# Kernel tuning notes

Measured on AMD Instinct MI355X. Metric: run time of the kernel, lower is better.

The kernel has to match this reference:

```python
import jax, jax.numpy as jnp
import numpy as np


def setup_inputs() -> dict:
    key = jax.random.key(0)
    ks = jax.random.split(key, 8)
    N, E, F, H = 50000, 400000, 128, 512
    x = jax.random.normal(ks[0], (N, F), dtype=jnp.float32)
    edge_index = jax.random.randint(ks[1], (2, E), 0, N, dtype=jnp.int32)
    W1 = jax.random.normal(ks[2], (H, 2 * F), dtype=jnp.float32) * 0.05
    b1 = jax.random.normal(ks[3], (H,), dtype=jnp.float32) * 0.05
    W2 = jax.random.normal(ks[4], (H, 2 * H), dtype=jnp.float32) * 0.05
    b2 = jax.random.normal(ks[5], (H,), dtype=jnp.float32) * 0.05
    Wo = jax.random.normal(ks[6], (1, H), dtype=jnp.float32) * 0.05
    bo = jax.random.normal(ks[7], (1,), dtype=jnp.float32) * 0.05
    return {"x": x, "edge_index": edge_index, "W1": W1, "b1": b1,
            "W2": W2, "b2": b2, "Wo": Wo, "bo": bo}


def reference(x, edge_index, W1, b1, W2, b2, Wo, bo):
    # GraphSAGE mean aggregation: agg[dst] = mean over incoming edges of h[src]
    N = x.shape[0]
    src = edge_index[0]
    dst = edge_index[1]
    deg = jax.ops.segment_sum(jnp.ones_like(dst, dtype=x.dtype), dst,
                              num_segments=N)
    inv_deg = 1.0 / jnp.maximum(deg, 1.0)  # clamp_min(1.0)

    def agg_mean(h):
        s = jax.ops.segment_sum(h[src], dst, num_segments=N)  # [N, D]
        return s * inv_deg[:, None]

    # Layer 1: concat(self, neigh) -> Linear -> ReLU (dropout = identity, eval)
    n1 = agg_mean(x)
    h1 = jax.nn.relu(jnp.concatenate([x, n1], axis=1) @ W1.T + b1)
    # Layer 2
    n2 = agg_mean(h1)
    h2 = jax.nn.relu(jnp.concatenate([h1, n2], axis=1) @ W2.T + b2)
    # Output head
    logits = h2 @ Wo.T + bo  # [N, 1]
    return jax.nn.sigmoid(logits)
```

## Files before the change

### kernel.cpp

```cpp
#include <hip/hip_runtime.h>
#include <math.h>


typedef __attribute__((ext_vector_type(8))) short bf16x8;
typedef __attribute__((ext_vector_type(4))) float f32x4;

static inline int ceil_div(int a, int b) { return (a + b - 1) / b; }

__device__ inline float bf2f_lo(unsigned u) { return __builtin_bit_cast(float, u << 16); }
__device__ inline float bf2f_hi(unsigned u) { return __builtin_bit_cast(float, u & 0xffff0000u); }
__device__ inline unsigned f2bf(float f) {
    unsigned u = __builtin_bit_cast(unsigned, f);
    u += 0x7fffu + ((u >> 16) & 1u);
    return u >> 16;
}

#define GLOAD_LDS16(gp, lp)                                                   \
    __builtin_amdgcn_global_load_lds(                                         \
        (__attribute__((address_space(1))) void*)(gp),                        \
        (__attribute__((address_space(3))) void*)(lp), 16, 0, 0)


__global__ void hist_kernel(const int* __restrict__ dst, int* __restrict__ deg, int E) {
    int e = blockIdx.x * 256 + threadIdx.x;
    if (e < E) atomicAdd(&deg[dst[e]], 1);
}

__global__ __launch_bounds__(256) void chunk_reduce(const int* __restrict__ deg,
                                                    int* __restrict__ partial, int N) {
    int base = blockIdx.x * 1024;
    int s = 0;
    for (int i = threadIdx.x; i < 1024; i += 256) {
        int idx = base + i;
        if (idx < N) s += deg[idx];
    }
    #pragma unroll
    for (int off = 32; off; off >>= 1) s += __shfl_down(s, off);
    __shared__ int ws[4];
    if ((threadIdx.x & 63) == 0) ws[threadIdx.x >> 6] = s;
    __syncthreads();
    if (threadIdx.x == 0) partial[blockIdx.x] = ws[0] + ws[1] + ws[2] + ws[3];
}

__global__ void partial_scan(int* __restrict__ partial, int* __restrict__ rowstartN, int P) {
    int lane = threadIdx.x;
    int v = (lane < P) ? partial[lane] : 0;
    int incl = v;
    #pragma unroll
    for (int off = 1; off < 64; off <<= 1) {
        int t = __shfl_up(incl, off);
        if (lane >= off) incl += t;
    }
    if (lane < P) partial[lane] = incl - v;
    if (lane == 63) *rowstartN = incl;
}

__global__ __launch_bounds__(256) void chunk_scan(const int* __restrict__ deg,
                                                  const int* __restrict__ partial,
                                                  int* __restrict__ rowstart,
                                                  int* __restrict__ cursor, int N) {
    int base = blockIdx.x * 1024 + threadIdx.x * 4;
    int v[4];
    #pragma unroll
    for (int j = 0; j < 4; ++j) {
        int i = base + j;
        v[j] = (i < N) ? deg[i] : 0;
    }
    int mysum = v[0] + v[1] + v[2] + v[3];
    int incl = mysum;
    int lane = threadIdx.x & 63, wave = threadIdx.x >> 6;
    #pragma unroll
    for (int off = 1; off < 64; off <<= 1) {
        int t = __shfl_up(incl, off);
        if (lane >= off) incl += t;
    }
    __shared__ int ws[4];
    if (lane == 63) ws[wave] = incl;
    __syncthreads();
    int run = partial[blockIdx.x] + incl - mysum;
    for (int w = 0; w < wave; ++w) run += ws[w];
    #pragma unroll
    for (int j = 0; j < 4; ++j) {
        int i = base + j;
        if (i < N) { rowstart[i] = run; cursor[i] = run; }
        run += v[j];
    }
}

__global__ void bucket_kernel(const int* __restrict__ src, const int* __restrict__ dst,
                              int* __restrict__ cursor, int* __restrict__ ebuf, int E) {
    int e = blockIdx.x * 256 + threadIdx.x;
    if (e < E) {
        int pos = atomicAdd(&cursor[dst[e]], 1);
        ebuf[pos] = src[e];
    }
}


__global__ void cvt_bf16_kernel(const float* __restrict__ in, unsigned short* __restrict__ out, int n4) {
    int i = blockIdx.x * 256 + threadIdx.x;
    if (i < n4) {
        float4 v = ((const float4*)in)[i];
        ushort4 o;
        o.x = (unsigned short)f2bf(v.x);
        o.y = (unsigned short)f2bf(v.y);
        o.z = (unsigned short)f2bf(v.z);
        o.w = (unsigned short)f2bf(v.w);
        ((ushort4*)out)[i] = o;
    }
}


__global__ void gather_mean_128(const int* __restrict__ rowstart, const int* __restrict__ ebuf,
                                const unsigned* __restrict__ featb, unsigned* __restrict__ outb, int N) {
    int w = (blockIdx.x * blockDim.x + threadIdx.x) >> 6;
    int lane = threadIdx.x & 63;
    if (w >= N) return;
    int e0 = rowstart[w], e1 = rowstart[w + 1];
    float ax = 0.0f, ay = 0.0f;
    int i = e0;
    for (; i + 4 <= e1; i += 4) {
        unsigned v0 = featb[(size_t)ebuf[i]     * 64 + lane];
        unsigned v1 = featb[(size_t)ebuf[i + 1] * 64 + lane];
        unsigned v2 = featb[(size_t)ebuf[i + 2] * 64 + lane];
        unsigned v3 = featb[(size_t)ebuf[i + 3] * 64 + lane];
        ax += bf2f_lo(v0) + bf2f_lo(v1) + bf2f_lo(v2) + bf2f_lo(v3);
        ay += bf2f_hi(v0) + bf2f_hi(v1) + bf2f_hi(v2) + bf2f_hi(v3);
    }
    for (; i < e1; ++i) {
        unsigned v = featb[(size_t)ebuf[i] * 64 + lane];
        ax += bf2f_lo(v); ay += bf2f_hi(v);
    }
    float inv = 1.0f / fmaxf((float)(e1 - e0), 1.0f);
    outb[(size_t)w * 64 + lane] = f2bf(ax * inv) | (f2bf(ay * inv) << 16);
}

__global__ void gather_mean_512(const int* __restrict__ rowstart, const int* __restrict__ ebuf,
                                const unsigned short* __restrict__ featb,
                                unsigned short* __restrict__ outb, int N) {
    int w = (blockIdx.x * blockDim.x + threadIdx.x) >> 6;
    int lane = threadIdx.x & 63;
    if (w >= N) return;
    int e0 = rowstart[w], e1 = rowstart[w + 1];
    float a[8] = {0, 0, 0, 0, 0, 0, 0, 0};
    const uint4* base = (const uint4*)featb;
    int i = e0;
    for (; i + 4 <= e1; i += 4) {
        uint4 v0 = base[(size_t)ebuf[i]     * 64 + lane];
        uint4 v1 = base[(size_t)ebuf[i + 1] * 64 + lane];
        uint4 v2 = base[(size_t)ebuf[i + 2] * 64 + lane];
        uint4 v3 = base[(size_t)ebuf[i + 3] * 64 + lane];
        a[0] += bf2f_lo(v0.x) + bf2f_lo(v1.x) + bf2f_lo(v2.x) + bf2f_lo(v3.x);
        a[1] += bf2f_hi(v0.x) + bf2f_hi(v1.x) + bf2f_hi(v2.x) + bf2f_hi(v3.x);
        a[2] += bf2f_lo(v0.y) + bf2f_lo(v1.y) + bf2f_lo(v2.y) + bf2f_lo(v3.y);
        a[3] += bf2f_hi(v0.y) + bf2f_hi(v1.y) + bf2f_hi(v2.y) + bf2f_hi(v3.y);
        a[4] += bf2f_lo(v0.z) + bf2f_lo(v1.z) + bf2f_lo(v2.z) + bf2f_lo(v3.z);
        a[5] += bf2f_hi(v0.z) + bf2f_hi(v1.z) + bf2f_hi(v2.z) + bf2f_hi(v3.z);
        a[6] += bf2f_lo(v0.w) + bf2f_lo(v1.w) + bf2f_lo(v2.w) + bf2f_lo(v3.w);
        a[7] += bf2f_hi(v0.w) + bf2f_hi(v1.w) + bf2f_hi(v2.w) + bf2f_hi(v3.w);
    }
    for (; i < e1; ++i) {
        uint4 v = base[(size_t)ebuf[i] * 64 + lane];
        a[0] += bf2f_lo(v.x); a[1] += bf2f_hi(v.x);
        a[2] += bf2f_lo(v.y); a[3] += bf2f_hi(v.y);
        a[4] += bf2f_lo(v.z); a[5] += bf2f_hi(v.z);
        a[6] += bf2f_lo(v.w); a[7] += bf2f_hi(v.w);
    }
    float inv = 1.0f / fmaxf((float)(e1 - e0), 1.0f);
    uint4 o;
    o.x = f2bf(a[0] * inv) | (f2bf(a[1] * inv) << 16);
    o.y = f2bf(a[2] * inv) | (f2bf(a[3] * inv) << 16);
    o.z = f2bf(a[4] * inv) | (f2bf(a[5] * inv) << 16);
    o.w = f2bf(a[6] * inv) | (f2bf(a[7] * inv) << 16);
    ((uint4*)outb)[(size_t)w * 64 + lane] = o;
}

__global__ __launch_bounds__(256) void gemm_mfma(
    const unsigned short* __restrict__ A0,
    const unsigned short* __restrict__ A1,
    const unsigned short* __restrict__ W,
    const float* __restrict__ b,
    unsigned short* __restrict__ outb,
    const float* __restrict__ Wo,
    float* __restrict__ logit,
    int N, int K0, int K1, int C, int mode)
{
    const int nrow = (N + 127) >> 7;
    const int id   = blockIdx.x;
    const int rowb = ((id >> 5) << 3) + (id & 7);
    const int colb = (id >> 3) & 3;
    if (rowb >= nrow) return;

    const int K = K0 + K1;
    const int S = K0;
    __shared__ short As[2][4096];
    __shared__ short Bs[2][4096];

    const int tid  = threadIdx.x;
    const int lane = tid & 63;
    const int wave = tid >> 6;
    const int wm = wave & 1, wn = wave >> 1;
    const int cl = lane & 15, quad = lane >> 4;
    const int row0 = rowb * 128;
    const int col0 = colb * 128;

    const int r = lane >> 2;
    const int j = lane & 3;
    const int trow0 = wave * 32 + r;
    const int trow1 = trow0 + 16;
    const int ar0 = (row0 + trow0 < N) ? row0 + trow0 : N - 1;
    const int ar1 = (row0 + trow1 < N) ? row0 + trow1 : N - 1;
    const size_t aoff0 = (size_t)ar0 * S + j * 8;
    const size_t aoff1 = (size_t)ar1 * S + j * 8;
    const size_t boff0 = (size_t)(col0 + trow0) * K + j * 8;
    const size_t boff1 = (size_t)(col0 + trow1) * K + j * 8;
    const int lds0 = (wave * 32) * 32;
    const int lds1 = (wave * 32 + 16) * 32;

    f32x4 acc[4][4];
    #pragma unroll
    for (int mt = 0; mt < 4; ++mt)
        #pragma unroll
        for (int nt = 0; nt < 4; ++nt)
            acc[mt][nt] = (f32x4){0.f, 0.f, 0.f, 0.f};

    GLOAD_LDS16(A0 + aoff0, &As[0][lds0]);
    GLOAD_LDS16(A0 + aoff1, &As[0][lds1]);
    GLOAD_LDS16(W  + boff0, &Bs[0][lds0]);
    GLOAD_LDS16(W  + boff1, &Bs[0][lds1]);

    const int iters = K >> 5;
    for (int i = 0; i < iters; ++i) {
        const int cur = i & 1;
        __syncthreads();
        if (i + 1 < iters) {
            const int kn = (i + 1) << 5;
            const unsigned short* Ab = (kn < K0) ? (A0 + kn) : (A1 + (kn - K0));
            const unsigned short* Wb = W + kn;
            const int nb = cur ^ 1;
            GLOAD_LDS16(Ab + aoff0, &As[nb][lds0]);
            GLOAD_LDS16(Ab + aoff1, &As[nb][lds1]);
            GLOAD_LDS16(Wb + boff0, &Bs[nb][lds0]);
            GLOAD_LDS16(Wb + boff1, &Bs[nb][lds1]);
        }

        bf16x8 af[4], bfr[4];
        #pragma unroll
        for (int mt = 0; mt < 4; ++mt)
            af[mt] = *(const bf16x8*)&As[cur][(wm * 64 + mt * 16 + cl) * 32 + quad * 8];
        #pragma unroll
        for (int nt = 0; nt < 4; ++nt)
            bfr[nt] = *(const bf16x8*)&Bs[cur][(wn * 64 + nt * 16 + cl) * 32 + quad * 8];

        #pragma unroll
        for (int mt = 0; mt < 4; ++mt)
            #pragma unroll
            for (int nt = 0; nt < 4; ++nt)
                acc[mt][nt] = __builtin_amdgcn_mfma_f32_16x16x32_bf16(
                    af[mt], bfr[nt], acc[mt][nt], 0, 0, 0);
    }

    if (mode == 0) {
        #pragma unroll
        for (int nt = 0; nt < 4; ++nt) {
            const int colx = col0 + wn * 64 + nt * 16 + cl;
            const float bb = b[colx];
            #pragma unroll
            for (int mt = 0; mt < 4; ++mt) {
                #pragma unroll
                for (int rr = 0; rr < 4; ++rr) {
                    int row = row0 + wm * 64 + mt * 16 + quad * 4 + rr;
                    if (row < N)
                        outb[(size_t)row * C + colx] =
                            (unsigned short)f2bf(fmaxf(acc[mt][nt][rr] + bb, 0.0f));
                }
            }
        }
    } else {
        float bv[4], wv2[4];
        #pragma unroll
        for (int nt = 0; nt < 4; ++nt) {
            const int colx = col0 + wn * 64 + nt * 16 + cl;
            bv[nt] = b[colx];
            wv2[nt] = Wo[colx];
        }
        #pragma unroll
        for (int mt = 0; mt < 4; ++mt) {
            #pragma unroll
            for (int rr = 0; rr < 4; ++rr) {
                float s = 0.0f;
                #pragma unroll
                for (int nt = 0; nt < 4; ++nt)
                    s += fmaxf(acc[mt][nt][rr] + bv[nt], 0.0f) * wv2[nt];
                s += __shfl_xor(s, 1);
                s += __shfl_xor(s, 2);
                s += __shfl_xor(s, 4);
                s += __shfl_xor(s, 8);
                int row = row0 + wm * 64 + mt * 16 + quad * 4 + rr;
                if (cl == 0 && row < N) atomicAdd(&logit[row], s);
            }
        }
    }
}

__global__ void head_kernel(const float* __restrict__ logit, const float* __restrict__ bo,
                            float* __restrict__ out, int N) {
    int i = blockIdx.x * 256 + threadIdx.x;
    if (i < N) out[i] = 1.0f / (1.0f + expf(-(logit[i] + bo[0])));
}

extern "C" void kernel_launch(void* const* d_in, const int* in_sizes, int n_in,
                              void* d_out, int out_size, void* d_ws, size_t ws_size,
                              hipStream_t stream) {
    const float* x  = (const float*)d_in[0];
    const int*   ei = (const int*)d_in[1];
    const float* W1 = (const float*)d_in[2];
    const float* b1 = (const float*)d_in[3];
    const float* W2 = (const float*)d_in[4];
    const float* b2 = (const float*)d_in[5];
    const float* Wo = (const float*)d_in[6];
    const float* bo = (const float*)d_in[7];
    float* out = (float*)d_out;

    const int N = in_sizes[0] / 128;
    const int E = in_sizes[1] / 2;
    const int* src = ei;
    const int* dst = ei + E;

    char* ws = (char*)d_ws;
    size_t off = 0;
    auto alloc = [&](size_t bytes) {
        void* p = ws + off;
        off += (bytes + 255) & ~(size_t)255;
        return p;
    };
    int* deg      = (int*)alloc((size_t)N * 4);
    int* rowstart = (int*)alloc((size_t)(N + 1) * 4);
    int* cursor   = (int*)alloc((size_t)N * 4);
    int* partial  = (int*)alloc((size_t)64 * 4);
    int* ebuf     = (int*)alloc((size_t)E * 4);
    float* logit  = (float*)alloc((size_t)N * 4);
    unsigned short* xb  = (unsigned short*)alloc((size_t)N * 128 * 2);
    unsigned short* W1b = (unsigned short*)alloc((size_t)512 * 256 * 2);
    unsigned short* W2b = (unsigned short*)alloc((size_t)512 * 1024 * 2);
    unsigned short* n1b = (unsigned short*)alloc((size_t)N * 128 * 2);
    unsigned short* h1b = (unsigned short*)alloc((size_t)N * 512 * 2);
    unsigned short* n2b = (unsigned short*)alloc((size_t)N * 512 * 2);
    (void)ws_size; (void)n_in; (void)out_size;

    hipMemsetAsync(deg,   0, (size_t)N * 4, stream);
    hipMemsetAsync(logit, 0, (size_t)N * 4, stream);

    cvt_bf16_kernel<<<ceil_div(N * 128 / 4, 256), 256, 0, stream>>>(x, xb, N * 128 / 4);
    cvt_bf16_kernel<<<ceil_div(512 * 256 / 4, 256), 256, 0, stream>>>(W1, W1b, 512 * 256 / 4);
    cvt_bf16_kernel<<<ceil_div(512 * 1024 / 4, 256), 256, 0, stream>>>(W2, W2b, 512 * 1024 / 4);

    const int P = ceil_div(N, 1024);
    hist_kernel<<<ceil_div(E, 256), 256, 0, stream>>>(dst, deg, E);
    chunk_reduce<<<P, 256, 0, stream>>>(deg, partial, N);
    partial_scan<<<1, 64, 0, stream>>>(partial, rowstart + N, P);
    chunk_scan<<<P, 256, 0, stream>>>(deg, partial, rowstart, cursor, N);
    bucket_kernel<<<ceil_div(E, 256), 256, 0, stream>>>(src, dst, cursor, ebuf, E);

    const int nrow = ceil_div(N, 128);
    const int gblocks = ceil_div(nrow, 8) * 8 * 4;

    gather_mean_128<<<ceil_div(N * 64, 256), 256, 0, stream>>>(rowstart, ebuf,
                                                               (const unsigned*)xb, (unsigned*)n1b, N);
    gemm_mfma<<<gblocks, 256, 0, stream>>>(xb, n1b, W1b, b1, h1b, nullptr, nullptr,
                                           N, 128, 128, 512, 0);

    gather_mean_512<<<ceil_div(N * 64, 256), 256, 0, stream>>>(rowstart, ebuf, h1b, n2b, N);
    gemm_mfma<<<gblocks, 256, 0, stream>>>(h1b, n2b, W2b, b2, nullptr, Wo, logit,
                                           N, 512, 512, 512, 1);

    head_kernel<<<ceil_div(N, 256), 256, 0, stream>>>(logit, bo, out, N);
}
```

Measured before the change: 352.8 us.

## Warp-specialize GEMM with producer waves and 5-stage LDS ring; fuse bf16 conversions

The MFMA GEMM is split into two producer waves that issue global-to-LDS loads three stages ahead into a five-slot ring, and two consumer waves that compute a 128x64 tile. Column tiles are halved and the grid doubled to match. The goal is to hide load latency behind MFMA work instead of relying on a two-stage double buffer. The three bf16 conversion launches are also merged into one kernel to save launch overhead. The trade-offs are half the waves doing math, more A reloads across column tiles, and a hand-coded waitcnt and barrier protocol whose correctness depends on the producer and consumer barrier counts matching.

After: 413.0 us. 17.1% more time.

```diff
diff --git a/kernel.cpp b/kernel.cpp
--- a/kernel.cpp
+++ b/kernel.cpp
@@ -19,6 +19,8 @@
     __builtin_amdgcn_global_load_lds(                                         \
         (__attribute__((address_space(1))) void*)(gp),                        \
         (__attribute__((address_space(3))) void*)(lp), 16, 0, 0)
+
+#define WAITCNT_VM18 0x4F72
 
 
 __global__ void hist_kernel(const int* __restrict__ dst, int* __restrict__ deg, int E) {
@@ -97,17 +99,22 @@
 }
 
 
-__global__ void cvt_bf16_kernel(const float* __restrict__ in, unsigned short* __restrict__ out, int n4) {
+__global__ void cvt3_bf16_kernel(const float* __restrict__ a, unsigned short* __restrict__ ao, int na4,
+                                 const float* __restrict__ b, unsigned short* __restrict__ bo, int nb4,
+                                 const float* __restrict__ c, unsigned short* __restrict__ co, int nc4) {
     int i = blockIdx.x * 256 + threadIdx.x;
-    if (i < n4) {
-        float4 v = ((const float4*)in)[i];
-        ushort4 o;
-        o.x = (unsigned short)f2bf(v.x);
-        o.y = (unsigned short)f2bf(v.y);
-        o.z = (unsigned short)f2bf(v.z);
-        o.w = (unsigned short)f2bf(v.w);
-        ((ushort4*)out)[i] = o;
-    }
+    const float* in; unsigned short* out; int k;
+    if (i < na4)                { in = a; out = ao; k = i; }
+    else if (i < na4 + nb4)     { in = b; out = bo; k = i - na4; }
+    else if (i < na4 + nb4 + nc4) { in = c; out = co; k = i - na4 - nb4; }
+    else return;
+    float4 v = ((const float4*)in)[k];
+    ushort4 o;
+    o.x = (unsigned short)f2bf(v.x);
+    o.y = (unsigned short)f2bf(v.y);
+    o.z = (unsigned short)f2bf(v.z);
+    o.w = (unsigned short)f2bf(v.w);
+    ((ushort4*)out)[k] = o;
 }
 
 
@@ -187,36 +194,67 @@
 {
     const int nrow = (N + 127) >> 7;
     const int id   = blockIdx.x;
-    const int rowb = ((id >> 5) << 3) + (id & 7);
-    const int colb = (id >> 3) & 3;
+    const int rowb = ((id >> 6) << 3) + (id & 7);
+    const int colb = (id >> 3) & 7;
     if (rowb >= nrow) return;
 
     const int K = K0 + K1;
     const int S = K0;
-    __shared__ short As[2][4096];
-    __shared__ short Bs[2][4096];
+    __shared__ short As[5][4096];
+    __shared__ short Bs[5][2048];
 
     const int tid  = threadIdx.x;
     const int lane = tid & 63;
     const int wave = tid >> 6;
-    const int wm = wave & 1, wn = wave >> 1;
+    const int row0 = rowb * 128;
+    const int col0 = colb * 64;
+    const int iters = K >> 5;
+
+    if (wave >= 2) {
+        const int p = wave - 2;
+        const int r = lane >> 2;
+        const int j = lane & 3;
+        size_t aoff[4], boff[2];
+        int lA[4], lB[2];
+        #pragma unroll
+        for (int q = 0; q < 4; ++q) {
+            int tr = p * 64 + q * 16 + r;
+            int ar = (row0 + tr < N) ? row0 + tr : N - 1;
+            aoff[q] = (size_t)ar * S + j * 8;
+            lA[q] = (p * 64 + q * 16) * 32;
+        }
+        #pragma unroll
+        for (int q = 0; q < 2; ++q) {
+            int tr = p * 32 + q * 16 + r;
+            boff[q] = (size_t)(col0 + tr) * K + j * 8;
+            lB[q] = (p * 32 + q * 16) * 32;
+        }
+        auto issue = [&](int t, int slot) {
+            const unsigned short* Ab = (t * 32 < K0) ? (A0 + t * 32)
+                                                     : (A1 + (t * 32 - K0));
+            const unsigned short* Wb = W + t * 32;
+            #pragma unroll
+            for (int q = 0; q < 4; ++q) GLOAD_LDS16(Ab + aoff[q], &As[slot][lA[q]]);
+            #pragma unroll
+            for (int q = 0; q < 2; ++q) GLOAD_LDS16(Wb + boff[q], &Bs[slot][lB[q]]);
+        };
+        issue(0, 0);
+        issue(1, 1);
+        issue(2, 2);
+        int slot = 3;
+        for (int i = 0; i < iters; ++i) {
+            int t = i + 3;
+            if (t > iters - 1) t = iters - 1;
+            issue(t, slot);
+            slot = (slot == 4) ? 0 : slot + 1;
+            __builtin_amdgcn_s_waitcnt(WAITCNT_VM18);
+            __builtin_amdgcn_s_barrier();
+        }
+        return;
+    }
+
+    const int wm = wave;
     const int cl = lane & 15, quad = lane >> 4;
-    const int row0 = rowb * 128;
-    const int col0 = colb * 128;
-
-    const int r = lane >> 2;
-    const int j = lane & 3;
-    const int trow0 = wave * 32 + r;
-    const int trow1 = trow0 + 16;
-    const int ar0 = (row0 + trow0 < N) ? row0 + trow0 : N - 1;
-    const int ar1 = (row0 + trow1 < N) ? row0 + trow1 : N - 1;
-    const size_t aoff0 = (size_t)ar0 * S + j * 8;
-    const size_t aoff1 = (size_t)ar1 * S + j * 8;
-    const size_t boff0 = (size_t)(col0 + trow0) * K + j * 8;
-    const size_t boff1 = (size_t)(col0 + trow1) * K + j * 8;
-    const int lds0 = (wave * 32) * 32;
-    const int lds1 = (wave * 32 + 16) * 32;
-
     f32x4 acc[4][4];
     #pragma unroll
     for (int mt = 0; mt < 4; ++mt)
@@ -224,46 +262,29 @@
         for (int nt = 0; nt < 4; ++nt)
             acc[mt][nt] = (f32x4){0.f, 0.f, 0.f, 0.f};
 
-    GLOAD_LDS16(A0 + aoff0, &As[0][lds0]);
-    GLOAD_LDS16(A0 + aoff1, &As[0][lds1]);
-    GLOAD_LDS16(W  + boff0, &Bs[0][lds0]);
-    GLOAD_LDS16(W  + boff1, &Bs[0][lds1]);
-
-    const int iters = K >> 5;
+    int slot = 0;
     for (int i = 0; i < iters; ++i) {
-        const int cur = i & 1;
         __syncthreads();
-        if (i + 1 < iters) {
-            const int kn = (i + 1) << 5;
-            const unsigned short* Ab = (kn < K0) ? (A0 + kn) : (A1 + (kn - K0));
-            const unsigned short* Wb = W + kn;
-            const int nb = cur ^ 1;
-            GLOAD_LDS16(Ab + aoff0, &As[nb][lds0]);
-            GLOAD_LDS16(Ab + aoff1, &As[nb][lds1]);
-            GLOAD_LDS16(Wb + boff0, &Bs[nb][lds0]);
-            GLOAD_LDS16(Wb + boff1, &Bs[nb][lds1]);
-        }
-
         bf16x8 af[4], bfr[4];
         #pragma unroll
         for (int mt = 0; mt < 4; ++mt)
-            af[mt] = *(const bf16x8*)&As[cur][(wm * 64 + mt * 16 + cl) * 32 + quad * 8];
+            af[mt] = *(const bf16x8*)&As[slot][(wm * 64 + mt * 16 + cl) * 32 + quad * 8];
         #pragma unroll
         for (int nt = 0; nt < 4; ++nt)
-            bfr[nt] = *(const bf16x8*)&Bs[cur][(wn * 64 + nt * 16 + cl) * 32 + quad * 8];
-
+            bfr[nt] = *(const bf16x8*)&Bs[slot][(nt * 16 + cl) * 32 + quad * 8];
         #pragma unroll
         for (int mt = 0; mt < 4; ++mt)
             #pragma unroll
             for (int nt = 0; nt < 4; ++nt)
                 acc[mt][nt] = __builtin_amdgcn_mfma_f32_16x16x32_bf16(
                     af[mt], bfr[nt], acc[mt][nt], 0, 0, 0);
+        slot = (slot == 4) ? 0 : slot + 1;
     }
 
     if (mode == 0) {
         #pragma unroll
         for (int nt = 0; nt < 4; ++nt) {
-            const int colx = col0 + wn * 64 + nt * 16 + cl;
+            const int colx = col0 + nt * 16 + cl;
             const float bb = b[colx];
             #pragma unroll
             for (int mt = 0; mt < 4; ++mt) {
@@ -280,7 +301,7 @@
         float bv[4], wv2[4];
         #pragma unroll
         for (int nt = 0; nt < 4; ++nt) {
-            const int colx = col0 + wn * 64 + nt * 16 + cl;
+            const int colx = col0 + nt * 16 + cl;
             bv[nt] = b[colx];
             wv2[nt] = Wo[colx];
         }
@@ -351,9 +372,9 @@
     hipMemsetAsync(deg,   0, (size_t)N * 4, stream);
     hipMemsetAsync(logit, 0, (size_t)N * 4, stream);
 
-    cvt_bf16_kernel<<<ceil_div(N * 128 / 4, 256), 256, 0, stream>>>(x, xb, N * 128 / 4);
-    cvt_bf16_kernel<<<ceil_div(512 * 256 / 4, 256), 256, 0, stream>>>(W1, W1b, 512 * 256 / 4);
-    cvt_bf16_kernel<<<ceil_div(512 * 1024 / 4, 256), 256, 0, stream>>>(W2, W2b, 512 * 1024 / 4);
+    const int na4 = N * 128 / 4, nb4 = 512 * 256 / 4, nc4 = 512 * 1024 / 4;
+    cvt3_bf16_kernel<<<ceil_div(na4 + nb4 + nc4, 256), 256, 0, stream>>>(
+        x, xb, na4, W1, W1b, nb4, W2, W2b, nc4);
 
     const int P = ceil_div(N, 1024);
     hist_kernel<<<ceil_div(E, 256), 256, 0, stream>>>(dst, deg, E);
@@ -363,7 +384,7 @@
     bucket_kernel<<<ceil_div(E, 256), 256, 0, stream>>>(src, dst, cursor, ebuf, E);
 
     const int nrow = ceil_div(N, 128);
-    const int gblocks = ceil_div(nrow, 8) * 8 * 4;
+    const int gblocks = ceil_div(nrow, 8) * 8 * 8;
 
     gather_mean_128<<<ceil_div(N * 64, 256), 256, 0, stream>>>(rowstart, ebuf,
                                                                (const unsigned*)xb, (unsigned*)n1b, N);
```
